# Performance work log

Hardware: AMD Instinct MI355X
Metric: run time of the kernel (lower is better)

## Reference

```python
import jax, jax.numpy as jnp
import numpy as np

N_NODES = 50000
E_EDGES = 800000
NEG_SLOPE = 0.2  # PyG GATConv LeakyReLU slope
BN_EPS = 1e-5


def _gat(x, src, dst, W, a_s, a_d, b, heads, ch, concat):
    """One GATConv (PyG semantics, eval mode): gather, per-edge attention,
    segment softmax over destination neighborhoods, scatter-add aggregation."""
    n = x.shape[0]
    h = (x @ W).reshape(n, heads, ch)                      # [N,H,C]
    es = jnp.sum(h * a_s, axis=-1)                         # [N,H] alpha_src per node
    ed = jnp.sum(h * a_d, axis=-1)                         # [N,H] alpha_dst per node
    e = jax.nn.leaky_relu(es[src] + ed[dst], NEG_SLOPE)    # [E,H] edge logits
    m = jax.ops.segment_max(e, dst, num_segments=n)        # stable segment softmax
    ex = jnp.exp(e - m[dst])
    den = jax.ops.segment_sum(ex, dst, num_segments=n)
    alpha = ex / den[dst]                                  # [E,H]
    out = jax.ops.segment_sum(h[src] * alpha[:, :, None], dst, num_segments=n)  # [N,H,C]
    out = out.reshape(n, heads * ch) if concat else out.mean(axis=1)
    return out + b


def _bn(x, g, b):
    # eval-mode BatchNorm1d with running_mean=0, running_var=1
    return x * (g / jnp.sqrt(1.0 + BN_EPS)) + b


def setup_inputs() -> dict:
    key = jax.random.key(0)
    k = jax.random.split(key, 24)
    s = 0.1
    inp = {
        "x": jax.random.normal(k[0], (N_NODES, 9), jnp.float32),
        "edge_index": jax.random.randint(k[1], (2, E_EDGES), 0, N_NODES, jnp.int32),
        "W1": jax.random.normal(k[2], (9, 512), jnp.float32) * s,
        "a1s": jax.random.normal(k[3], (8, 64), jnp.float32) * s,
        "a1d": jax.random.normal(k[4], (8, 64), jnp.float32) * s,
        "b1": jax.random.normal(k[5], (512,), jnp.float32) * s,
        "W2": jax.random.normal(k[6], (512, 128), jnp.float32) * s,
        "a2s": jax.random.normal(k[7], (4, 32), jnp.float32) * s,
        "a2d": jax.random.normal(k[8], (4, 32), jnp.float32) * s,
        "b2": jax.random.normal(k[9], (128,), jnp.float32) * s,
        "W3": jax.random.normal(k[10], (128, 32), jnp.float32) * s,
        "a3s": jax.random.normal(k[11], (1, 32), jnp.float32) * s,
        "a3d": jax.random.normal(k[12], (1, 32), jnp.float32) * s,
        "b3": jax.random.normal(k[13], (32,), jnp.float32) * s,
        "g1": jax.random.uniform(k[14], (512,), jnp.float32, 0.5, 1.5),
        "be1": jax.random.normal(k[15], (512,), jnp.float32) * s,
        "g2": jax.random.uniform(k[16], (128,), jnp.float32, 0.5, 1.5),
        "be2": jax.random.normal(k[17], (128,), jnp.float32) * s,
        "g3": jax.random.uniform(k[18], (32,), jnp.float32, 0.5, 1.5),
        "be3": jax.random.normal(k[19], (32,), jnp.float32) * s,
        "Wh": jax.random.normal(k[20], (32, 1), jnp.float32) * s,
        "bh": jax.random.normal(k[21], (1,), jnp.float32) * s,
    }
    return inp


def reference(x, edge_index, W1, a1s, a1d, b1, W2, a2s, a2d, b2,
              W3, a3s, a3d, b3, g1, be1, g2, be2, g3, be3, Wh, bh):
    n = x.shape[0]
    loops = jnp.arange(n, dtype=edge_index.dtype)          # PyG add_self_loops=True
    src = jnp.concatenate([edge_index[0], loops])
    dst = jnp.concatenate([edge_index[1], loops])
    h = _gat(x, src, dst, W1, a1s, a1d, b1, heads=8, ch=64, concat=True)
    h = jax.nn.elu(_bn(h, g1, be1))
    h = _gat(h, src, dst, W2, a2s, a2d, b2, heads=4, ch=32, concat=True)
    h = jax.nn.elu(_bn(h, g2, be2))
    h = _gat(h, src, dst, W3, a3s, a3d, b3, heads=1, ch=32, concat=False)
    h = jax.nn.elu(_bn(h, g3, be3))
    return h @ Wh + bh                                     # [N,1]
```

## Files before the change

### kernel.cpp

```cpp
#include <hip/hip_runtime.h>
#include <hip/hip_bf16.h>
#include <math.h>

#define N_NODES 50000
#define E_EDGES 800000
#define ET (E_EDGES + N_NODES)
#define NBLK_SCAN ((N_NODES + 255) / 256)
#define MPAD 50048
#define NPB_T1 16

typedef __attribute__((ext_vector_type(8))) short bf16x8;
typedef __attribute__((ext_vector_type(4))) float f32x4;
typedef __attribute__((ext_vector_type(8))) _Float16 half8;


__global__ void zero_int_kernel(int* __restrict__ p, int n) {
    int i = blockIdx.x * blockDim.x + threadIdx.x;
    if (i < n) p[i] = 0;
}

__global__ void hist_kernel(const int* __restrict__ ei, int* __restrict__ cnt) {
    int e = blockIdx.x * blockDim.x + threadIdx.x;
    if (e < ET) {
        int d = (e < E_EDGES) ? ei[E_EDGES + e] : (e - E_EDGES);
        atomicAdd(&cnt[d], 1);
    }
}

__global__ void scan1_kernel(const int* __restrict__ cnt, int* __restrict__ rp,
                             int* __restrict__ bsum) {
    __shared__ int s[256];
    int i = blockIdx.x * 256 + threadIdx.x;
    int v = (i < N_NODES) ? cnt[i] : 0;
    s[threadIdx.x] = v;
    __syncthreads();
    for (int off = 1; off < 256; off <<= 1) {
        int t = (threadIdx.x >= off) ? s[threadIdx.x - off] : 0;
        __syncthreads();
        s[threadIdx.x] += t;
        __syncthreads();
    }
    if (i < N_NODES) rp[i + 1] = s[threadIdx.x];
    if (threadIdx.x == 255) bsum[blockIdx.x] = s[255];
}

__global__ void scan2_kernel(int* __restrict__ bsum, int nb) {
    __shared__ int s[256];
    int v = (threadIdx.x < nb) ? bsum[threadIdx.x] : 0;
    s[threadIdx.x] = v;
    __syncthreads();
    for (int off = 1; off < 256; off <<= 1) {
        int t = (threadIdx.x >= off) ? s[threadIdx.x - off] : 0;
        __syncthreads();
        s[threadIdx.x] += t;
        __syncthreads();
    }
    if (threadIdx.x < nb) bsum[threadIdx.x] = (threadIdx.x == 0) ? 0 : s[threadIdx.x - 1];
}

__global__ void scan3_kernel(int* __restrict__ rp, const int* __restrict__ bsum,
                             int* __restrict__ cursor) {
    int i = blockIdx.x * 256 + threadIdx.x;
    if (i == 0) rp[0] = 0;
    if (i < N_NODES) {
        int incl = rp[i + 1] + bsum[i >> 8];
        rp[i + 1] = incl;
        cursor[i] = incl - cursor[i];
    }
}

__global__ void fill_kernel(const int* __restrict__ ei, int* __restrict__ cursor,
                            int* __restrict__ col) {
    int e = blockIdx.x * blockDim.x + threadIdx.x;
    if (e < ET) {
        int s_, d;
        if (e < E_EDGES) { s_ = ei[e]; d = ei[E_EDGES + e]; }
        else             { s_ = e - E_EDGES; d = s_; }
        int p = atomicAdd(&cursor[d], 1);
        col[p] = s_;
    }
}


__global__ void prep_attn1_kernel(const float* __restrict__ W1,
                                  const float* __restrict__ a1s,
                                  const float* __restrict__ a1d,
                                  float* __restrict__ M) {
    int t = threadIdx.x;
    if (t < 144) {
        int which = t / 72, idx = t % 72, k = idx / 8, h = idx % 8;
        const float* a = which ? a1d : a1s;
        float s = 0.f;
        for (int c = 0; c < 64; c++) s += W1[k * 512 + h * 64 + c] * a[h * 64 + c];
        M[t] = s;
    }
}

__global__ void es_ed1_kernel(const float* __restrict__ x, const float* __restrict__ M,
                              float* __restrict__ es, float* __restrict__ ed) {
    int n = blockIdx.x * blockDim.x + threadIdx.x;
    if (n >= N_NODES) return;
    float xr[9];
#pragma unroll
    for (int k = 0; k < 9; k++) xr[k] = x[(size_t)n * 9 + k];
#pragma unroll
    for (int h = 0; h < 8; h++) {
        float s1 = 0.f, s2 = 0.f;
#pragma unroll
        for (int k = 0; k < 9; k++) {
            s1 += xr[k] * M[k * 8 + h];
            s2 += xr[k] * M[72 + k * 8 + h];
        }
        es[(size_t)n * 8 + h] = s1;
        ed[(size_t)n * 8 + h] = s2;
    }
}

__global__ __launch_bounds__(128) void agg1_kernel(const float* __restrict__ x,
        const int* __restrict__ rp, const int* __restrict__ col,
        const float* __restrict__ es, const float* __restrict__ ed,
        float* __restrict__ aggx) {
    __shared__ int   s_src[64];
    __shared__ float s_x[64][9];
    __shared__ float s_es[64][8];
    __shared__ float s_w[8][64];
    __shared__ float s_m[8], s_den[8], s_scale[8], s_ed[8];
    int n = blockIdx.x, tid = threadIdx.x;
    int start = rp[n], end = rp[n + 1];
    if (tid < 8) { s_m[tid] = -INFINITY; s_den[tid] = 0.f; s_ed[tid] = ed[(size_t)n * 8 + tid]; }
    __syncthreads();
    float acc = 0.f;
    int ghh = tid >> 4, glane = tid & 15;
    for (int cs = start; cs < end; cs += 64) {
        int cnt = min(64, end - cs);
        if (tid < cnt) s_src[tid] = col[cs + tid];
        __syncthreads();
        for (int q = tid; q < cnt * 9; q += 128) {
            int e = q / 9, k = q - e * 9;
            s_x[e][k] = x[(size_t)s_src[e] * 9 + k];
        }
        for (int q = tid; q < cnt * 8; q += 128) {
            int e = q >> 3, h = q & 7;
            s_es[e][h] = es[(size_t)s_src[e] * 8 + h];
        }
        __syncthreads();
        float lmax = -INFINITY;
        for (int e = glane; e < cnt; e += 16) {
            float l = s_es[e][ghh] + s_ed[ghh];
            l = (l > 0.f) ? l : 0.2f * l;
            s_w[ghh][e] = l;
            lmax = fmaxf(lmax, l);
        }
#pragma unroll
        for (int off = 8; off > 0; off >>= 1) lmax = fmaxf(lmax, __shfl_xor(lmax, off));
        float mold = s_m[ghh];
        float nm = fmaxf(mold, lmax);
        float fac = __expf(mold - nm);
        float psum = 0.f;
        for (int e = glane; e < cnt; e += 16) {
            float w = __expf(s_w[ghh][e] - nm);
            s_w[ghh][e] = w;
            psum += w;
        }
#pragma unroll
        for (int off = 8; off > 0; off >>= 1) psum += __shfl_xor(psum, off);
        if (glane == 0) { s_den[ghh] = s_den[ghh] * fac + psum; s_m[ghh] = nm; s_scale[ghh] = fac; }
        __syncthreads();
        if (tid < 72) {
            int hh = tid / 9, k = tid - hh * 9;
            float a = acc * s_scale[hh];
            for (int e = 0; e < cnt; e++) a += s_w[hh][e] * s_x[e][k];
            acc = a;
        }
        __syncthreads();
    }
    if (tid < 72) {
        int hh = tid / 9;
        aggx[(size_t)n * 72 + tid] = acc / s_den[hh];
    }
}

__global__ __launch_bounds__(256) void transform1_kernel(const float* __restrict__ aggx,
        const float* __restrict__ W1, const float* __restrict__ b1,
        const float* __restrict__ g1, const float* __restrict__ be1,
        __hip_bfloat16* __restrict__ Ah, __hip_bfloat16* __restrict__ Al) {
    __shared__ float s_a[NPB_T1 * 72];
    int tid = threadIdx.x;
    int n0 = blockIdx.x * NPB_T1;
    int nn = min(NPB_T1, N_NODES - n0);
    for (int q = tid; q < nn * 72; q += 256) s_a[q] = aggx[(size_t)n0 * 72 + q];
    int c0 = tid * 2;
    int hh = c0 >> 6;
    float2 wv[9];
#pragma unroll
    for (int k = 0; k < 9; k++) wv[k] = *(const float2*)&W1[k * 512 + c0];
    float2 bv = *(const float2*)&b1[c0];
    float2 gv = *(const float2*)&g1[c0];
    float2 ev = *(const float2*)&be1[c0];
    float gs0 = gv.x / sqrtf(1.00001f), gs1 = gv.y / sqrtf(1.00001f);
    __syncthreads();
    for (int i = 0; i < nn; i++) {
        const float* ar = &s_a[i * 72 + hh * 9];
        float v0 = bv.x, v1 = bv.y;
#pragma unroll
        for (int k = 0; k < 9; k++) { float a = ar[k]; v0 += a * wv[k].x; v1 += a * wv[k].y; }
        v0 = v0 * gs0 + ev.x;
        v1 = v1 * gs1 + ev.y;
        v0 = (v0 > 0.f) ? v0 : expm1f(v0);
        v1 = (v1 > 0.f) ? v1 : expm1f(v1);
        __hip_bfloat16 h0 = __float2bfloat16(v0), h1 = __float2bfloat16(v1);
        float r0 = v0 - __bfloat162float(h0), r1 = v1 - __bfloat162float(h1);
        size_t base = (size_t)(n0 + i) * 512 + c0;
        __hip_bfloat162 hp; hp.x = h0; hp.y = h1;
        __hip_bfloat162 lp; lp.x = __float2bfloat16(r0); lp.y = __float2bfloat16(r1);
        *(__hip_bfloat162*)&Ah[base] = hp;
        *(__hip_bfloat162*)&Al[base] = lp;
    }
}

__global__ void prep_w2_kernel(const float* __restrict__ W2,
                               __hip_bfloat16* __restrict__ Wh,
                               __hip_bfloat16* __restrict__ Wl) {
    int t = blockIdx.x * 256 + threadIdx.x;
    if (t < 512 * 128) {
        int k = t >> 7, c = t & 127;
        float v = W2[t];
        __hip_bfloat16 hi = __float2bfloat16(v);
        float r = v - __bfloat162float(hi);
        Wh[c * 512 + k] = hi;
        Wl[c * 512 + k] = __float2bfloat16(r);
    }
}


__global__ __launch_bounds__(256) void gemm2_mfma_kernel(
        const __hip_bfloat16* __restrict__ Ah, const __hip_bfloat16* __restrict__ Al,
        const __hip_bfloat16* __restrict__ Wh, const __hip_bfloat16* __restrict__ Wl,
        _Float16* __restrict__ C) {
    __shared__ short lds[32768];
    int tid = threadIdx.x;
    int wv = tid >> 6;
    int lane = tid & 63;
    int lrow = lane & 15, kgrp = lane >> 4;
    int m0 = blockIdx.x * 128;

    f32x4 acc[2][8];
#pragma unroll
    for (int m = 0; m < 2; m++)
#pragma unroll
        for (int n = 0; n < 8; n++) acc[m][n] = (f32x4){0.f, 0.f, 0.f, 0.f};

    for (int kk = 0; kk < 512; kk += 64) {
#pragma unroll
        for (int tI = 0; tI < 4; tI++) {
            const __hip_bfloat16* src = (tI == 0) ? Ah : (tI == 1) ? Al : (tI == 2) ? Wh : Wl;
            int rowBase = (tI < 2) ? m0 : 0;
#pragma unroll
            for (int i = 0; i < 4; i++) {
                int gid = tid + 256 * i;
                int row = gid >> 3, kg = gid & 7;
                bf16x8 v = *(const bf16x8*)(src + (size_t)(rowBase + row) * 512 + kk + kg * 8);
                *(bf16x8*)(lds + tI * 8192 + row * 64 + ((kg ^ (row & 7)) << 3)) = v;
            }
        }
        __syncthreads();
#pragma unroll
        for (int ks = 0; ks < 2; ks++) {
            bf16x8 ah[2], al[2];
#pragma unroll
            for (int m = 0; m < 2; m++) {
                int row = wv * 32 + m * 16 + lrow;
                int kg = ks * 4 + kgrp;
                int so = row * 64 + ((kg ^ (row & 7)) << 3);
                ah[m] = *(const bf16x8*)(lds + so);
                al[m] = *(const bf16x8*)(lds + 8192 + so);
            }
#pragma unroll
            for (int n = 0; n < 8; n++) {
                int colr = n * 16 + lrow;
                int kg = ks * 4 + kgrp;
                int so = colr * 64 + ((kg ^ (colr & 7)) << 3);
                bf16x8 wh = *(const bf16x8*)(lds + 16384 + so);
                bf16x8 wl = *(const bf16x8*)(lds + 24576 + so);
#pragma unroll
                for (int m = 0; m < 2; m++) {
                    acc[m][n] = __builtin_amdgcn_mfma_f32_16x16x32_bf16(ah[m], wh, acc[m][n], 0, 0, 0);
                    acc[m][n] = __builtin_amdgcn_mfma_f32_16x16x32_bf16(al[m], wh, acc[m][n], 0, 0, 0);
                    acc[m][n] = __builtin_amdgcn_mfma_f32_16x16x32_bf16(ah[m], wl, acc[m][n], 0, 0, 0);
                }
            }
        }
        __syncthreads();
    }
#pragma unroll
    for (int m = 0; m < 2; m++) {
#pragma unroll
        for (int n = 0; n < 8; n++) {
#pragma unroll
            for (int r = 0; r < 4; r++) {
                int row = m0 + wv * 32 + m * 16 + (lane >> 4) * 4 + r;
                int colc = n * 16 + (lane & 15);
                if (row < N_NODES) C[(size_t)row * 128 + colc] = (_Float16)acc[m][n][r];
            }
        }
    }
}


template <int H, int C>
__global__ void attn_dots_h_kernel(const _Float16* __restrict__ hin,
                                   const float* __restrict__ as_, const float* __restrict__ ad_,
                                   float* __restrict__ es, float* __restrict__ ed) {
    int t = blockIdx.x * blockDim.x + threadIdx.x;
    if (t >= N_NODES * H) return;
    int n = t / H, hh = t % H;
    const half8* row = (const half8*)(hin + (size_t)n * (H * C) + hh * C);
    float s1 = 0.f, s2 = 0.f;
#pragma unroll
    for (int c8 = 0; c8 < C / 8; c8++) {
        half8 v = row[c8];
#pragma unroll
        for (int j = 0; j < 8; j++) {
            float f = (float)v[j];
            s1 += f * as_[hh * C + c8 * 8 + j];
            s2 += f * ad_[hh * C + c8 * 8 + j];
        }
    }
    es[t] = s1;
    ed[t] = s2;
}


__global__ __launch_bounds__(64) void agg2_fused_kernel(
        const _Float16* __restrict__ hin,
        const int* __restrict__ rp, const int* __restrict__ col,
        const float* __restrict__ es, const float* __restrict__ ed,
        const float* __restrict__ b2, const float* __restrict__ g2,
        const float* __restrict__ be2,
        const float* __restrict__ W3, const float* __restrict__ a3s,
        const float* __restrict__ a3d,
        _Float16* __restrict__ h3, float* __restrict__ es3, float* __restrict__ ed3) {
    constexpr int H = 4, HC = 128, LPH = 16, G = 4, CH = 64;
    __shared__ int   s_src[CH];
    __shared__ float s_w[H][CH];
    __shared__ float s_red[G][HC];
    __shared__ float s_res[HC];
    __shared__ float s_m[H], s_den[H], s_scale[H], s_ed[H];

    int n = blockIdx.x, tid = threadIdx.x;
    int start = rp[n], end = rp[n + 1];
    if (tid < H) { s_m[tid] = -INFINITY; s_den[tid] = 0.f; s_ed[tid] = ed[(size_t)n * H + tid]; }
    __syncthreads();

    int ghh = tid >> 4, glane = tid & 15;
    int g = tid >> 4, rl = tid & 15;
    int hh2 = rl >> 2;
    float a0[8], a1[8];
#pragma unroll
    for (int j = 0; j < 8; j++) { a0[j] = 0.f; a1[j] = 0.f; }

    for (int cs = start; cs < end; cs += CH) {
        int cnt = min(CH, end - cs);
        if (tid < cnt) s_src[tid] = col[cs + tid];
        __syncthreads();

        {
            float lmax = -INFINITY;
            for (int e = glane; e < cnt; e += LPH) {
                float l = es[(size_t)s_src[e] * H + ghh] + s_ed[ghh];
                l = (l > 0.f) ? l : 0.2f * l;
                s_w[ghh][e] = l;
                lmax = fmaxf(lmax, l);
            }
#pragma unroll
            for (int off = 8; off > 0; off >>= 1) lmax = fmaxf(lmax, __shfl_xor(lmax, off));
            float mold = s_m[ghh];
            float nm = fmaxf(mold, lmax);
            float fac = __expf(mold - nm);
            float psum = 0.f;
            for (int e = glane; e < cnt; e += LPH) {
                float w = __expf(s_w[ghh][e] - nm);
                s_w[ghh][e] = w;
                psum += w;
            }
#pragma unroll
            for (int off = 8; off > 0; off >>= 1) psum += __shfl_xor(psum, off);
            if (glane == 0) { s_den[ghh] = s_den[ghh] * fac + psum; s_m[ghh] = nm; s_scale[ghh] = fac; }
        }
        __syncthreads();

        {
            float fac = s_scale[hh2];
#pragma unroll
            for (int j = 0; j < 8; j++) a0[j] *= fac;
            int e = g;
            for (; e + G < cnt; e += 2 * G) {
                float w0 = s_w[hh2][e];
                float w1 = s_w[hh2][e + G];
                half8 v0 = *(const half8*)&hin[(size_t)s_src[e] * HC + rl * 8];
                half8 v1 = *(const half8*)&hin[(size_t)s_src[e + G] * HC + rl * 8];
#pragma unroll
                for (int j = 0; j < 8; j++) a0[j] += w0 * (float)v0[j];
#pragma unroll
                for (int j = 0; j < 8; j++) a1[j] += w1 * (float)v1[j];
            }
            if (e < cnt) {
                float w0 = s_w[hh2][e];
                half8 v0 = *(const half8*)&hin[(size_t)s_src[e] * HC + rl * 8];
#pragma unroll
                for (int j = 0; j < 8; j++) a0[j] += w0 * (float)v0[j];
            }
        }
        __syncthreads();
    }

#pragma unroll
    for (int j = 0; j < 8; j++) s_red[g][rl * 8 + j] = a0[j] + a1[j];
    __syncthreads();

    const float rsq = 0.99999499f;
#pragma unroll
    for (int half = 0; half < 2; half++) {
        int c = tid + half * 64;
        float r = s_red[0][c] + s_red[1][c] + s_red[2][c] + s_red[3][c];
        r /= s_den[c >> 5];
        r += b2[c];
        r = r * (g2[c] * rsq) + be2[c];
        r = (r > 0.f) ? r : expm1f(r);
        s_res[c] = r;
    }
    __syncthreads();

    int halfk = tid >> 5, j = tid & 31;
    float v = 0.f;
#pragma unroll 16
    for (int c = halfk * 64; c < halfk * 64 + 64; c++) v += s_res[c] * W3[c * 32 + j];
    v += __shfl_xor(v, 32);
    if (tid < 32) h3[(size_t)n * 32 + j] = (_Float16)v;
    float p1 = v * a3s[j], p2 = v * a3d[j];
#pragma unroll
    for (int off = 16; off > 0; off >>= 1) {
        p1 += __shfl_xor(p1, off);
        p2 += __shfl_xor(p2, off);
    }
    if (tid == 0) { es3[n] = p1; ed3[n] = p2; }
}


__global__ __launch_bounds__(64) void agg3_fused_kernel(
        const _Float16* __restrict__ hin,
        const int* __restrict__ rp, const int* __restrict__ col,
        const float* __restrict__ es3, const float* __restrict__ ed3,
        const float* __restrict__ b3, const float* __restrict__ g3,
        const float* __restrict__ be3,
        const float* __restrict__ Wh, const float* __restrict__ bh,
        float* __restrict__ out) {
    constexpr int G = 16, CH = 64;
    __shared__ int   s_src[CH];
    __shared__ float s_w[CH];
    __shared__ float s_red[G][32];
    __shared__ float s_m1, s_den1, s_scale1, s_ed1;

    int n = blockIdx.x, tid = threadIdx.x;
    int start = rp[n], end = rp[n + 1];
    if (tid == 0) { s_m1 = -INFINITY; s_den1 = 0.f; s_ed1 = ed3[n]; }
    __syncthreads();

    int g = tid >> 2, rl = tid & 3;
    float a0[8], a1[8];
#pragma unroll
    for (int j = 0; j < 8; j++) { a0[j] = 0.f; a1[j] = 0.f; }

    for (int cs = start; cs < end; cs += CH) {
        int cnt = min(CH, end - cs);
        if (tid < cnt) s_src[tid] = col[cs + tid];
        __syncthreads();

        float lmax = -INFINITY;
        float l = 0.f;
        if (tid < cnt) {
            l = es3[s_src[tid]] + s_ed1;
            l = (l > 0.f) ? l : 0.2f * l;
            lmax = l;
        }
#pragma unroll
        for (int off = 32; off > 0; off >>= 1) lmax = fmaxf(lmax, __shfl_xor(lmax, off));
        float mold = s_m1;
        float nm = fmaxf(mold, lmax);
        float fac = __expf(mold - nm);
        float w = 0.f;
        if (tid < cnt) {
            w = __expf(l - nm);
            s_w[tid] = w;
        }
        float psum = w;
#pragma unroll
        for (int off = 32; off > 0; off >>= 1) psum += __shfl_xor(psum, off);
        if (tid == 0) { s_den1 = s_den1 * fac + psum; s_m1 = nm; s_scale1 = fac; }
        __syncthreads();

        {
#pragma unroll
            for (int j = 0; j < 8; j++) a0[j] *= fac;
            int e = g;
            for (; e + G < cnt; e += 2 * G) {
                float w0 = s_w[e];
                float w1 = s_w[e + G];
                half8 v0 = *(const half8*)&hin[(size_t)s_src[e] * 32 + rl * 8];
                half8 v1 = *(const half8*)&hin[(size_t)s_src[e + G] * 32 + rl * 8];
#pragma unroll
                for (int j = 0; j < 8; j++) a0[j] += w0 * (float)v0[j];
#pragma unroll
                for (int j = 0; j < 8; j++) a1[j] += w1 * (float)v1[j];
            }
            if (e < cnt) {
                float w0 = s_w[e];
                half8 v0 = *(const half8*)&hin[(size_t)s_src[e] * 32 + rl * 8];
#pragma unroll
                for (int j = 0; j < 8; j++) a0[j] += w0 * (float)v0[j];
            }
        }
        __syncthreads();
    }

#pragma unroll
    for (int j = 0; j < 8; j++) s_red[g][rl * 8 + j] = a0[j] + a1[j];
    __syncthreads();

    const float rsq = 0.99999499f;
    float p = 0.f;
    if (tid < 32) {
        float r = 0.f;
#pragma unroll
        for (int q = 0; q < G; q++) r += s_red[q][tid];
        r /= s_den1;
        r += b3[tid];
        r = r * (g3[tid] * rsq) + be3[tid];
        r = (r > 0.f) ? r : expm1f(r);
        p = r * Wh[tid];
    }
#pragma unroll
    for (int off = 16; off > 0; off >>= 1) p += __shfl_xor(p, off);
    if (tid == 0) out[n] = p + bh[0];
}


extern "C" void kernel_launch(void* const* d_in, const int* in_sizes, int n_in,
                              void* d_out, int out_size, void* d_ws, size_t ws_size,
                              hipStream_t stream) {
    const float* x   = (const float*)d_in[0];
    const int*   ei  = (const int*)d_in[1];
    const float* W1  = (const float*)d_in[2];
    const float* a1s = (const float*)d_in[3];
    const float* a1d = (const float*)d_in[4];
    const float* b1  = (const float*)d_in[5];
    const float* W2  = (const float*)d_in[6];
    const float* a2s = (const float*)d_in[7];
    const float* a2d = (const float*)d_in[8];
    const float* b2  = (const float*)d_in[9];
    const float* W3  = (const float*)d_in[10];
    const float* a3s = (const float*)d_in[11];
    const float* a3d = (const float*)d_in[12];
    const float* b3  = (const float*)d_in[13];
    const float* g1  = (const float*)d_in[14];
    const float* be1 = (const float*)d_in[15];
    const float* g2  = (const float*)d_in[16];
    const float* be2 = (const float*)d_in[17];
    const float* g3  = (const float*)d_in[18];
    const float* be3 = (const float*)d_in[19];
    const float* Wh  = (const float*)d_in[20];
    const float* bh  = (const float*)d_in[21];
    float* out = (float*)d_out;

    char* ws = (char*)d_ws;
    size_t off = 0;
    auto alloc = [&](size_t bytes) -> void* {
        void* p = ws + off;
        off += (bytes + 255) & ~(size_t)255;
        return p;
    };
    int*   row_ptr = (int*)alloc((N_NODES + 1) * sizeof(int));
    int*   cursor  = (int*)alloc((N_NODES + 1) * sizeof(int));
    int*   bsum    = (int*)alloc(256 * sizeof(int));
    int*   col_src = (int*)alloc((size_t)ET * sizeof(int));
    float* es      = (float*)alloc((size_t)N_NODES * 8 * sizeof(float));
    float* ed      = (float*)alloc((size_t)N_NODES * 8 * sizeof(float));
    float* es3     = (float*)alloc((size_t)N_NODES * sizeof(float));
    float* ed3     = (float*)alloc((size_t)N_NODES * sizeof(float));
    float* bufA    = (float*)alloc((size_t)N_NODES * 72 * sizeof(float));
    _Float16* h2h  = (_Float16*)alloc((size_t)N_NODES * 128 * sizeof(_Float16));
    _Float16* h3h  = (_Float16*)alloc((size_t)N_NODES * 32 * sizeof(_Float16));
    __hip_bfloat16* Ah   = (__hip_bfloat16*)alloc((size_t)MPAD * 512 * sizeof(__hip_bfloat16));
    __hip_bfloat16* Al   = (__hip_bfloat16*)alloc((size_t)MPAD * 512 * sizeof(__hip_bfloat16));
    __hip_bfloat16* W2Th = (__hip_bfloat16*)alloc((size_t)128 * 512 * sizeof(__hip_bfloat16));
    __hip_bfloat16* W2Tl = (__hip_bfloat16*)alloc((size_t)128 * 512 * sizeof(__hip_bfloat16));
    float* M1 = (float*)(ws + ((ws_size - 1024) & ~(size_t)255));
    float* aggx = bufA;

    zero_int_kernel<<<(N_NODES + 1 + 255) / 256, 256, 0, stream>>>(cursor, N_NODES + 1);
    hist_kernel<<<(ET + 255) / 256, 256, 0, stream>>>(ei, cursor);
    scan1_kernel<<<NBLK_SCAN, 256, 0, stream>>>(cursor, row_ptr, bsum);
    scan2_kernel<<<1, 256, 0, stream>>>(bsum, NBLK_SCAN);
    scan3_kernel<<<NBLK_SCAN, 256, 0, stream>>>(row_ptr, bsum, cursor);
    fill_kernel<<<(ET + 255) / 256, 256, 0, stream>>>(ei, cursor, col_src);

    prep_attn1_kernel<<<1, 256, 0, stream>>>(W1, a1s, a1d, M1);
    es_ed1_kernel<<<(N_NODES + 255) / 256, 256, 0, stream>>>(x, M1, es, ed);
    agg1_kernel<<<N_NODES, 128, 0, stream>>>(x, row_ptr, col_src, es, ed, aggx);
    transform1_kernel<<<(N_NODES + NPB_T1 - 1) / NPB_T1, 256, 0, stream>>>(aggx, W1, b1, g1, be1, Ah, Al);

    prep_w2_kernel<<<256, 256, 0, stream>>>(W2, W2Th, W2Tl);
    gemm2_mfma_kernel<<<MPAD / 128, 256, 0, stream>>>(Ah, Al, W2Th, W2Tl, h2h);
    attn_dots_h_kernel<4, 32><<<(N_NODES * 4 + 255) / 256, 256, 0, stream>>>(h2h, a2s, a2d, es, ed);
    agg2_fused_kernel<<<N_NODES, 64, 0, stream>>>(h2h, row_ptr, col_src, es, ed,
                                                  b2, g2, be2, W3, a3s, a3d,
                                                  h3h, es3, ed3);

    agg3_fused_kernel<<<N_NODES, 64, 0, stream>>>(h3h, row_ptr, col_src, es3, ed3,
                                                  b3, g3, be3, Wh, bh, out);
}
```

Before: 411.0 us.

## Use single fp16 MFMA GEMM with fused attention-logit columns, drop bf16 split

Layer-2 GEMM now uses one fp16 operand instead of a bf16 hi/lo split with three MFMAs per tile. This halves the A-matrix traffic and cuts MFMA work to a third. The attention source/destination dot products are folded into the GEMM as 8 extra weight columns (W2·a precomputed), which removes the separate attn_dots kernel. W3 is pre-transposed so agg2 can do float4 dot products, and the shared reduction arrays are padded against bank conflicts. The trade-off is lower precision: fp16 activations lose range and mantissa compared with the split-bf16 scheme, and the logits now come from fp16-rounded folded weights.

After: 432.6 us. 5.3% more time.

```diff
diff --git a/kernel.cpp b/kernel.cpp
--- a/kernel.cpp
+++ b/kernel.cpp
@@ -8,10 +8,11 @@
 #define NBLK_SCAN ((N_NODES + 255) / 256)
 #define MPAD 50048
 #define NPB_T1 16
-
-typedef __attribute__((ext_vector_type(8))) short bf16x8;
+#define WROWS 160
+
 typedef __attribute__((ext_vector_type(4))) float f32x4;
 typedef __attribute__((ext_vector_type(8))) _Float16 half8;
+typedef __attribute__((ext_vector_type(2))) _Float16 half2v;
 
 
 __global__ void zero_int_kernel(int* __restrict__ p, int n) {
@@ -183,7 +184,7 @@
 __global__ __launch_bounds__(256) void transform1_kernel(const float* __restrict__ aggx,
         const float* __restrict__ W1, const float* __restrict__ b1,
         const float* __restrict__ g1, const float* __restrict__ be1,
-        __hip_bfloat16* __restrict__ Ah, __hip_bfloat16* __restrict__ Al) {
+        _Float16* __restrict__ Af) {
     __shared__ float s_a[NPB_T1 * 72];
     int tid = threadIdx.x;
     int n0 = blockIdx.x * NPB_T1;
@@ -208,86 +209,87 @@
         v1 = v1 * gs1 + ev.y;
         v0 = (v0 > 0.f) ? v0 : expm1f(v0);
         v1 = (v1 > 0.f) ? v1 : expm1f(v1);
-        __hip_bfloat16 h0 = __float2bfloat16(v0), h1 = __float2bfloat16(v1);
-        float r0 = v0 - __bfloat162float(h0), r1 = v1 - __bfloat162float(h1);
-        size_t base = (size_t)(n0 + i) * 512 + c0;
-        __hip_bfloat162 hp; hp.x = h0; hp.y = h1;
-        __hip_bfloat162 lp; lp.x = __float2bfloat16(r0); lp.y = __float2bfloat16(r1);
-        *(__hip_bfloat162*)&Ah[base] = hp;
-        *(__hip_bfloat162*)&Al[base] = lp;
-    }
-}
-
-__global__ void prep_w2_kernel(const float* __restrict__ W2,
-                               __hip_bfloat16* __restrict__ Wh,
-                               __hip_bfloat16* __restrict__ Wl) {
+        half2v hp;
+        hp[0] = (_Float16)v0;
+        hp[1] = (_Float16)v1;
+        *(half2v*)&Af[(size_t)(n0 + i) * 512 + c0] = hp;
+    }
+}
+
+__global__ void prep2_kernel(const float* __restrict__ W2,
+                             const float* __restrict__ a2s, const float* __restrict__ a2d,
+                             const float* __restrict__ W3,
+                             _Float16* __restrict__ WT, float* __restrict__ W3T) {
     int t = blockIdx.x * 256 + threadIdx.x;
-    if (t < 512 * 128) {
+    if (t < 65536) {
         int k = t >> 7, c = t & 127;
-        float v = W2[t];
-        __hip_bfloat16 hi = __float2bfloat16(v);
-        float r = v - __bfloat162float(hi);
-        Wh[c * 512 + k] = hi;
-        Wl[c * 512 + k] = __float2bfloat16(r);
+        WT[(size_t)c * 512 + k] = (_Float16)W2[t];
+    } else if (t < 65536 + 4096) {
+        int q = t - 65536;
+        int hd8 = q >> 9, k = q & 511;
+        const float* a = (hd8 < 4) ? a2s : a2d;
+        int hd = hd8 & 3;
+        float s = 0.f;
+#pragma unroll
+        for (int c = 0; c < 32; c++) s += W2[k * 128 + hd * 32 + c] * a[hd * 32 + c];
+        WT[(size_t)(128 + hd8) * 512 + k] = (_Float16)s;
+    } else if (t < 65536 + 4096 + 4096) {
+        int q = t - 65536 - 4096;
+        int c = q >> 5, j = q & 31;
+        W3T[j * 128 + c] = W3[q];
     }
 }
 
 
 __global__ __launch_bounds__(256) void gemm2_mfma_kernel(
-        const __hip_bfloat16* __restrict__ Ah, const __hip_bfloat16* __restrict__ Al,
-        const __hip_bfloat16* __restrict__ Wh, const __hip_bfloat16* __restrict__ Wl,
-        _Float16* __restrict__ C) {
-    __shared__ short lds[32768];
+        const _Float16* __restrict__ A, const _Float16* __restrict__ WT,
+        _Float16* __restrict__ h2, float* __restrict__ es, float* __restrict__ ed) {
+    __shared__ _Float16 ldsA[128 * 64];
+    __shared__ _Float16 ldsW[WROWS * 64];
     int tid = threadIdx.x;
     int wv = tid >> 6;
     int lane = tid & 63;
     int lrow = lane & 15, kgrp = lane >> 4;
     int m0 = blockIdx.x * 128;
 
-    f32x4 acc[2][8];
+    f32x4 acc[2][9];
 #pragma unroll
     for (int m = 0; m < 2; m++)
 #pragma unroll
-        for (int n = 0; n < 8; n++) acc[m][n] = (f32x4){0.f, 0.f, 0.f, 0.f};
+        for (int n = 0; n < 9; n++) acc[m][n] = (f32x4){0.f, 0.f, 0.f, 0.f};
 
     for (int kk = 0; kk < 512; kk += 64) {
 #pragma unroll
-        for (int tI = 0; tI < 4; tI++) {
-            const __hip_bfloat16* src = (tI == 0) ? Ah : (tI == 1) ? Al : (tI == 2) ? Wh : Wl;
-            int rowBase = (tI < 2) ? m0 : 0;
-#pragma unroll
-            for (int i = 0; i < 4; i++) {
-                int gid = tid + 256 * i;
-                int row = gid >> 3, kg = gid & 7;
-                bf16x8 v = *(const bf16x8*)(src + (size_t)(rowBase + row) * 512 + kk + kg * 8);
-                *(bf16x8*)(lds + tI * 8192 + row * 64 + ((kg ^ (row & 7)) << 3)) = v;
-            }
+        for (int i = 0; i < 4; i++) {
+            int gid = tid + 256 * i;
+            int row = gid >> 3, kg = gid & 7;
+            half8 v = *(const half8*)(A + (size_t)(m0 + row) * 512 + kk + kg * 8);
+            *(half8*)(ldsA + row * 64 + ((kg ^ (row & 7)) << 3)) = v;
+        }
+#pragma unroll
+        for (int i = 0; i < 5; i++) {
+            int gid = tid + 256 * i;
+            int row = gid >> 3, kg = gid & 7;
+            half8 v = *(const half8*)(WT + (size_t)row * 512 + kk + kg * 8);
+            *(half8*)(ldsW + row * 64 + ((kg ^ (row & 7)) << 3)) = v;
         }
         __syncthreads();
 #pragma unroll
         for (int ks = 0; ks < 2; ks++) {
-            bf16x8 ah[2], al[2];
+            int kg = ks * 4 + kgrp;
+            half8 af[2];
 #pragma unroll
             for (int m = 0; m < 2; m++) {
                 int row = wv * 32 + m * 16 + lrow;
-                int kg = ks * 4 + kgrp;
-                int so = row * 64 + ((kg ^ (row & 7)) << 3);
-                ah[m] = *(const bf16x8*)(lds + so);
-                al[m] = *(const bf16x8*)(lds + 8192 + so);
-            }
-#pragma unroll
-            for (int n = 0; n < 8; n++) {
+                af[m] = *(const half8*)(ldsA + row * 64 + ((kg ^ (row & 7)) << 3));
+            }
+#pragma unroll
+            for (int n = 0; n < 9; n++) {
                 int colr = n * 16 + lrow;
-                int kg = ks * 4 + kgrp;
-                int so = colr * 64 + ((kg ^ (colr & 7)) << 3);
-                bf16x8 wh = *(const bf16x8*)(lds + 16384 + so);
-                bf16x8 wl = *(const bf16x8*)(lds + 24576 + so);
-#pragma unroll
-                for (int m = 0; m < 2; m++) {
-                    acc[m][n] = __builtin_amdgcn_mfma_f32_16x16x32_bf16(ah[m], wh, acc[m][n], 0, 0, 0);
-                    acc[m][n] = __builtin_amdgcn_mfma_f32_16x16x32_bf16(al[m], wh, acc[m][n], 0, 0, 0);
-                    acc[m][n] = __builtin_amdgcn_mfma_f32_16x16x32_bf16(ah[m], wl, acc[m][n], 0, 0, 0);
-                }
+                half8 wf = *(const half8*)(ldsW + colr * 64 + ((kg ^ (colr & 7)) << 3));
+#pragma unroll
+                for (int m = 0; m < 2; m++)
+                    acc[m][n] = __builtin_amdgcn_mfma_f32_16x16x32_f16(af[m], wf, acc[m][n], 0, 0, 0);
             }
         }
         __syncthreads();
@@ -295,39 +297,17 @@
 #pragma unroll
     for (int m = 0; m < 2; m++) {
 #pragma unroll
-        for (int n = 0; n < 8; n++) {
-#pragma unroll
-            for (int r = 0; r < 4; r++) {
-                int row = m0 + wv * 32 + m * 16 + (lane >> 4) * 4 + r;
-                int colc = n * 16 + (lane & 15);
-                if (row < N_NODES) C[(size_t)row * 128 + colc] = (_Float16)acc[m][n][r];
-            }
-        }
-    }
-}
-
-
-template <int H, int C>
-__global__ void attn_dots_h_kernel(const _Float16* __restrict__ hin,
-                                   const float* __restrict__ as_, const float* __restrict__ ad_,
-                                   float* __restrict__ es, float* __restrict__ ed) {
-    int t = blockIdx.x * blockDim.x + threadIdx.x;
-    if (t >= N_NODES * H) return;
-    int n = t / H, hh = t % H;
-    const half8* row = (const half8*)(hin + (size_t)n * (H * C) + hh * C);
-    float s1 = 0.f, s2 = 0.f;
-#pragma unroll
-    for (int c8 = 0; c8 < C / 8; c8++) {
-        half8 v = row[c8];
-#pragma unroll
-        for (int j = 0; j < 8; j++) {
-            float f = (float)v[j];
-            s1 += f * as_[hh * C + c8 * 8 + j];
-            s2 += f * ad_[hh * C + c8 * 8 + j];
-        }
-    }
-    es[t] = s1;
-    ed[t] = s2;
+        for (int r = 0; r < 4; r++) {
+            int row = m0 + wv * 32 + m * 16 + (lane >> 4) * 4 + r;
+            if (row < N_NODES) {
+#pragma unroll
+                for (int n = 0; n < 8; n++)
+                    h2[(size_t)row * 128 + n * 16 + lrow] = (_Float16)acc[m][n][r];
+                if (lrow < 4)      es[(size_t)row * 4 + lrow]     = acc[m][8][r];
+                else if (lrow < 8) ed[(size_t)row * 4 + lrow - 4] = acc[m][8][r];
+            }
+        }
+    }
 }
 
 
@@ -337,13 +317,13 @@
         const float* __restrict__ es, const float* __restrict__ ed,
         const float* __restrict__ b2, const float* __restrict__ g2,
         const float* __restrict__ be2,
-        const float* __restrict__ W3, const float* __restrict__ a3s,
+        const float* __restrict__ W3T, const float* __restrict__ a3s,
         const float* __restrict__ a3d,
         _Float16* __restrict__ h3, float* __restrict__ es3, float* __restrict__ ed3) {
     constexpr int H = 4, HC = 128, LPH = 16, G = 4, CH = 64;
     __shared__ int   s_src[CH];
     __shared__ float s_w[H][CH];
-    __shared__ float s_red[G][HC];
+    __shared__ float s_red[G][HC + 4];
     __shared__ float s_res[HC];
     __shared__ float s_m[H], s_den[H], s_scale[H], s_ed[H];
 
@@ -414,8 +394,13 @@
         __syncthreads();
     }
 
-#pragma unroll
-    for (int j = 0; j < 8; j++) s_red[g][rl * 8 + j] = a0[j] + a1[j];
+    {
+        float4 p0, p1;
+        p0.x = a0[0] + a1[0]; p0.y = a0[1] + a1[1]; p0.z = a0[2] + a1[2]; p0.w = a0[3] + a1[3];
+        p1.x = a0[4] + a1[4]; p1.y = a0[5] + a1[5]; p1.z = a0[6] + a1[6]; p1.w = a0[7] + a1[7];
+        *(float4*)&s_red[g][rl * 8]     = p0;
+        *(float4*)&s_red[g][rl * 8 + 4] = p1;
+    }
     __syncthreads();
 
     const float rsq = 0.99999499f;
@@ -432,18 +417,23 @@
     __syncthreads();
 
     int halfk = tid >> 5, j = tid & 31;
+    const float4* s4 = (const float4*)&s_res[halfk * 64];
+    const float4* w4 = (const float4*)&W3T[j * 128 + halfk * 64];
     float v = 0.f;
-#pragma unroll 16
-    for (int c = halfk * 64; c < halfk * 64 + 64; c++) v += s_res[c] * W3[c * 32 + j];
+#pragma unroll
+    for (int c4 = 0; c4 < 16; c4++) {
+        float4 a = s4[c4], b = w4[c4];
+        v += a.x * b.x + a.y * b.y + a.z * b.z + a.w * b.w;
+    }
     v += __shfl_xor(v, 32);
     if (tid < 32) h3[(size_t)n * 32 + j] = (_Float16)v;
-    float p1 = v * a3s[j], p2 = v * a3d[j];
+    float p1s = v * a3s[j], p2s = v * a3d[j];
 #pragma unroll
     for (int off = 16; off > 0; off >>= 1) {
-        p1 += __shfl_xor(p1, off);
-        p2 += __shfl_xor(p2, off);
-    }
-    if (tid == 0) { es3[n] = p1; ed3[n] = p2; }
+        p1s += __shfl_xor(p1s, off);
+        p2s += __shfl_xor(p2s, off);
+    }
+    if (tid == 0) { es3[n] = p1s; ed3[n] = p2s; }
 }
 
 
@@ -458,7 +448,7 @@
     constexpr int G = 16, CH = 64;
     __shared__ int   s_src[CH];
     __shared__ float s_w[CH];
-    __shared__ float s_red[G][32];
+    __shared__ float s_red[G][36];
     __shared__ float s_m1, s_den1, s_scale1, s_ed1;
 
     int n = blockIdx.x, tid = threadIdx.x;
@@ -587,15 +577,13 @@
     float* ed      = (float*)alloc((size_t)N_NODES * 8 * sizeof(float));
     float* es3     = (float*)alloc((size_t)N_NODES * sizeof(float));
     float* ed3     = (float*)alloc((size_t)N_NODES * sizeof(float));
-    float* bufA    = (float*)alloc((size_t)N_NODES * 72 * sizeof(float));
+    float* aggx    = (float*)alloc((size_t)N_NODES * 72 * sizeof(float));
     _Float16* h2h  = (_Float16*)alloc((size_t)N_NODES * 128 * sizeof(_Float16));
     _Float16* h3h  = (_Float16*)alloc((size_t)N_NODES * 32 * sizeof(_Float16));
-    __hip_bfloat16* Ah   = (__hip_bfloat16*)alloc((size_t)MPAD * 512 * sizeof(__hip_bfloat16));
-    __hip_bfloat16* Al   = (__hip_bfloat16*)alloc((size_t)MPAD * 512 * sizeof(__hip_bfloat16));
-    __hip_bfloat16* W2Th = (__hip_bfloat16*)alloc((size_t)128 * 512 * sizeof(__hip_bfloat16));
-    __hip_bfloat16* W2Tl = (__hip_bfloat16*)alloc((size_t)128 * 512 * sizeof(__hip_bfloat16));
+    _Float16* Af   = (_Float16*)alloc((size_t)MPAD * 512 * sizeof(_Float16));
+    _Float16* WT   = (_Float16*)alloc((size_t)WROWS * 512 * sizeof(_Float16));
+    float* W3T     = (float*)alloc(32 * 128 * sizeof(float));
     float* M1 = (float*)(ws + ((ws_size - 1024) & ~(size_t)255));
-    float* aggx = bufA;
 
     zero_int_kernel<<<(N_NODES + 1 + 255) / 256, 256, 0, stream>>>(cursor, N_NODES + 1);
     hist_kernel<<<(ET + 255) / 256, 256, 0, stream>>>(ei, cursor);
@@ -607,13 +595,12 @@
     prep_attn1_kernel<<<1, 256, 0, stream>>>(W1, a1s, a1d, M1);
     es_ed1_kernel<<<(N_NODES + 255) / 256, 256, 0, stream>>>(x, M1, es, ed);
     agg1_kernel<<<N_NODES, 128, 0, stream>>>(x, row_ptr, col_src, es, ed, aggx);
-    transform1_kernel<<<(N_NODES + NPB_T1 - 1) / NPB_T1, 256, 0, stream>>>(aggx, W1, b1, g1, be1, Ah, Al);
-
-    prep_w2_kernel<<<256, 256, 0, stream>>>(W2, W2Th, W2Tl);
-    gemm2_mfma_kernel<<<MPAD / 128, 256, 0, stream>>>(Ah, Al, W2Th, W2Tl, h2h);
-    attn_dots_h_kernel<4, 32><<<(N_NODES * 4 + 255) / 256, 256, 0, stream>>>(h2h, a2s, a2d, es, ed);
+    transform1_kernel<<<(N_NODES + NPB_T1 - 1) / NPB_T1, 256, 0, stream>>>(aggx, W1, b1, g1, be1, Af);
+
+    prep2_kernel<<<288, 256, 0, stream>>>(W2, a2s, a2d, W3, WT, W3T);
+    gemm2_mfma_kernel<<<MPAD / 128, 256, 0, stream>>>(Af, WT, h2h, es, ed);
     agg2_fused_kernel<<<N_NODES, 64, 0, stream>>>(h2h, row_ptr, col_src, es, ed,
-                                                  b2, g2, be2, W3, a3s, a3d,
+                                                  b2, g2, be2, W3T, a3s, a3d,
                                                   h3h, es3, ed3);
 
     agg3_fused_kernel<<<N_NODES, 64, 0, stream>>>(h3h, row_ptr, col_src, es3, ed3,
```
